# Performance work log

Hardware: AMD Instinct MI355X
Metric: run time of the kernel (lower is better)

The kernel has to match this reference:

```python
import jax, jax.numpy as jnp
import numpy as np

B, S, D = 4, 2048, 1024
P = 9            # num_paths
DM = D // 4      # bottleneck d_mid
EPS = 1e-5


def setup_inputs() -> dict:
    key = jax.random.key(0)
    ks = jax.random.split(key, 12)
    sc_in = 1.0 / np.sqrt(D)
    sc_mid = 1.0 / np.sqrt(DM)
    return {
        "x": jax.random.normal(ks[0], (B, S, D), dtype=jnp.float32),
        # neighbor mixer: per-channel 3-tap kernel over the sequence axis
        "mix_kernel": jax.random.normal(ks[1], (3, D), dtype=jnp.float32) * 0.5,
        # 9 parallel bottleneck paths: D -> D/4 -> D
        "W1": jax.random.normal(ks[2], (P, D, DM), dtype=jnp.float32) * sc_in,
        "b1": jnp.zeros((P, DM), dtype=jnp.float32),
        "W2": jax.random.normal(ks[3], (P, DM, D), dtype=jnp.float32) * sc_mid,
        "b2": jnp.zeros((P, D), dtype=jnp.float32),
        # observer: D -> D/4 -> tanh -> ... -> P scores
        "Wo1": jax.random.normal(ks[4], (D, DM), dtype=jnp.float32) * sc_in,
        "bo1": jnp.zeros((DM,), dtype=jnp.float32),
        "Wo2": jax.random.normal(ks[5], (DM, P), dtype=jnp.float32) * sc_mid,
        "bo2": jnp.zeros((P,), dtype=jnp.float32),
        # output norm affine params
        "gamma": jnp.ones((D,), dtype=jnp.float32),
        "beta": jnp.zeros((D,), dtype=jnp.float32),
    }


def _mix(x, mix_kernel):
    # eidosNeighborMixer: local 3-tap depthwise mix along sequence (non-causal)
    xp = jnp.pad(x, ((0, 0), (1, 1), (0, 0)))
    return (mix_kernel[0] * xp[:, :-2]
            + mix_kernel[1] * xp[:, 1:-1]
            + mix_kernel[2] * xp[:, 2:])


def _layernorm(h, gamma, beta):
    mu = jnp.mean(h, axis=-1, keepdims=True)
    var = jnp.var(h, axis=-1, keepdims=True)
    return (h - mu) * jax.lax.rsqrt(var + EPS) * gamma + beta


def reference(x, mix_kernel, W1, b1, W2, b2, Wo1, bo1, Wo2, bo2, gamma, beta):
    x_mixed = _mix(x, mix_kernel)                                   # [B,S,D]
    # all num_paths bottleneck transforms computed densely (as in source)
    h = jnp.einsum("bsd,pdm->bspm", x_mixed, W1) + b1               # [B,S,P,DM]
    stacked_paths = jnp.einsum("bspm,pmd->bspd", h, W2) + b2        # [B,S,P,D]
    # observer scores
    scores = jnp.tanh(x_mixed @ Wo1 + bo1) @ Wo2 + bo2              # [B,S,P]
    # eval-mode collapse: hard argmax one-hot selection
    idx = jnp.argmax(scores, axis=-1)                               # [B,S]
    weights = jax.nn.one_hot(idx, P, dtype=stacked_paths.dtype)     # [B,S,P]
    collapsed = jnp.einsum("bspd,bsp->bsd", stacked_paths, weights)  # [B,S,D]
    return _layernorm(x + collapsed, gamma, beta)
```

## Files before the change

kernel.cpp:

```cpp
#include <hip/hip_runtime.h>
#include <math.h>

#define Ss 2048
#define Dd 1024
#define Pp 9
#define DMm 256
#define Tt 8192
#define EPSf 1e-5f
#define BAND 6e-3f

typedef __attribute__((ext_vector_type(8))) __bf16 bf16x8;
typedef __attribute__((ext_vector_type(4))) float f32x4;

#define GLOBAL_AS __attribute__((address_space(1)))
#define LDS_AS __attribute__((address_space(3)))

#define MAXTILES 137

__device__ __forceinline__ unsigned short bf16rn(float f) {
  unsigned int u = __float_as_uint(f);
  unsigned int r = (u + 0x7fffu + ((u >> 16) & 1u)) >> 16;
  return (unsigned short)r;
}

__device__ __forceinline__ void gload16(const void* g, void* l) {
  __builtin_amdgcn_global_load_lds((const GLOBAL_AS unsigned int*)g,
                                   (LDS_AS unsigned int*)l, 16, 0, 0);
}

#define KSW(r, sl) (((r) << 6) + ((((sl) ^ ((r) & 7))) << 3))

__global__ __launch_bounds__(256) void k_mix2(const float* __restrict__ x,
    const float* __restrict__ mk, unsigned short* __restrict__ xh,
    int* __restrict__ counts) {
  if (blockIdx.x == 0 && threadIdx.x < 64) counts[threadIdx.x] = 0;
  const int t = blockIdx.x;
  const int s = t & (Ss - 1);
  const int d = threadIdx.x << 2;
  const float* xc = x + (size_t)t * Dd + d;
  float4 vb = *(const float4*)xc;
  float4 va = make_float4(0.f, 0.f, 0.f, 0.f);
  float4 vc = make_float4(0.f, 0.f, 0.f, 0.f);
  if (s > 0)      va = *(const float4*)(xc - Dd);
  if (s < Ss - 1) vc = *(const float4*)(xc + Dd);
  const float4 k0 = *(const float4*)(mk + d);
  const float4 k1 = *(const float4*)(mk + Dd + d);
  const float4 k2 = *(const float4*)(mk + 2 * Dd + d);
  float4 o;
  o.x = k0.x * va.x + k1.x * vb.x + k2.x * vc.x;
  o.y = k0.y * va.y + k1.y * vb.y + k2.y * vc.y;
  o.z = k0.z * va.z + k1.z * vb.z + k2.z * vc.z;
  o.w = k0.w * va.w + k1.w * vb.w + k2.w * vc.w;
  ushort4 h;
  h.x = bf16rn(o.x); h.y = bf16rn(o.y); h.z = bf16rn(o.z); h.w = bf16rn(o.w);
  *(ushort4*)(xh + (size_t)t * Dd + d) = h;
}

__global__ __launch_bounds__(256) void k_cvt_all(
    const float* __restrict__ W1, const float* __restrict__ W2,
    const float* __restrict__ Wo1,
    unsigned short* __restrict__ W1t, unsigned short* __restrict__ W2t,
    unsigned short* __restrict__ Wo1t) {
  const int z = blockIdx.z;
  const float* in; unsigned short* outp; int R, C, r0, c0;
  if (z < Pp)            { in = W1;  outp = W1t;  R = Dd;  C = DMm;
                           r0 = blockIdx.x * 32; c0 = blockIdx.y * 32; }
  else if (z < 2 * Pp)   { in = W2;  outp = W2t;  R = DMm; C = Dd;
                           r0 = blockIdx.y * 32; c0 = blockIdx.x * 32; }
  else                   { in = Wo1; outp = Wo1t; R = Dd;  C = DMm;
                           r0 = blockIdx.x * 32; c0 = blockIdx.y * 32; }
  const int zi = (z < Pp) ? z : ((z < 2 * Pp) ? z - Pp : 0);
  const size_t zo = (size_t)zi * R * C;
  __shared__ float tile[32][33];
  const int tr = threadIdx.x >> 3, tc = (threadIdx.x & 7) << 2;
  float4 v = *(const float4*)(in + zo + (size_t)(r0 + tr) * C + c0 + tc);
  tile[tr][tc] = v.x; tile[tr][tc + 1] = v.y; tile[tr][tc + 2] = v.z; tile[tr][tc + 3] = v.w;
  __syncthreads();
  ushort4 h;
  h.x = bf16rn(tile[tc + 0][tr]); h.y = bf16rn(tile[tc + 1][tr]);
  h.z = bf16rn(tile[tc + 2][tr]); h.w = bf16rn(tile[tc + 3][tr]);
  *(ushort4*)(outp + zo + (size_t)(c0 + tr) * R + r0 + tc) = h;
}

template<int KTOT, int NTOT, int MODE, bool GROUPED>
__global__ __launch_bounds__(256) void k_gemm(
    const unsigned short* __restrict__ A,
    const unsigned short* __restrict__ Bt,
    const float* __restrict__ bias,
    const float* __restrict__ resid,
    float* __restrict__ outf, unsigned short* __restrict__ outh,
    const int* __restrict__ counts, const int* __restrict__ tokenlist) {
  int p = 0, ti = blockIdx.x, cnt = Tt;
  if (GROUPED) {
    for (p = 0; p < Pp; ++p) {
      cnt = counts[p];
      const int nt = (cnt + 63) >> 6;
      if (ti < nt) break;
      ti -= nt;
    }
    if (p == Pp) return;
  }
  const int tile0 = ti * 64;
  __shared__ int tl[64];
  __shared__ __align__(16) unsigned short As[2][64 * 64];
  __shared__ __align__(16) unsigned short Bs[2][128 * 64];
  const int tid = threadIdx.x;
  if (tid < 64) {
    const int li = tile0 + tid;
    if (GROUPED) tl[tid] = (li < cnt) ? tokenlist[p * Tt + li] : tokenlist[p * Tt];
    else         tl[tid] = li;
  }
  __syncthreads();
  const int w = tid >> 6, lane = tid & 63;
  const int fr = lane & 15, fs = lane >> 4;
  const int wr = w >> 1, wc = w & 1;
  const int n0 = blockIdx.y * 128;
  const unsigned short* Bp0 = Bt + (size_t)p * NTOT * KTOT + (size_t)n0 * KTOT;
  const unsigned short* srcA[2];
  #pragma unroll
  for (int i = 0; i < 2; ++i) {
    const int u = i * 256 + tid, r = u >> 3, sl = (u & 7) ^ (r & 7);
    srcA[i] = A + (size_t)tl[r] * KTOT + sl * 8;
  }
  const unsigned short* srcB[4];
  #pragma unroll
  for (int i = 0; i < 4; ++i) {
    const int u = i * 256 + tid, r = u >> 3, sl = (u & 7) ^ (r & 7);
    srcB[i] = Bp0 + (size_t)r * KTOT + sl * 8;
  }
  const int ldsW = w * 512;
  int aoff[2][2], boff[4][2];
  #pragma unroll
  for (int m = 0; m < 2; ++m)
    #pragma unroll
    for (int kk = 0; kk < 2; ++kk)
      aoff[m][kk] = KSW(wr * 32 + m * 16 + fr, kk * 4 + fs);
  #pragma unroll
  for (int n = 0; n < 4; ++n)
    #pragma unroll
    for (int kk = 0; kk < 2; ++kk)
      boff[n][kk] = KSW(wc * 64 + n * 16 + fr, kk * 4 + fs);

#define STAGE(b, kb) do { \
    gload16(srcA[0] + (kb), &As[b][0] + ldsW); \
    gload16(srcA[1] + (kb), &As[b][0] + 2048 + ldsW); \
    gload16(srcB[0] + (kb), &Bs[b][0] + ldsW); \
    gload16(srcB[1] + (kb), &Bs[b][0] + 2048 + ldsW); \
    gload16(srcB[2] + (kb), &Bs[b][0] + 4096 + ldsW); \
    gload16(srcB[3] + (kb), &Bs[b][0] + 6144 + ldsW); \
  } while (0)

  f32x4 acc[2][4] = {};
  const int NS = KTOT / 64;
  STAGE(0, 0);
  for (int s = 0; s < NS; ++s) {
    const int buf = s & 1;
    if (s + 1 < NS) {
      STAGE(buf ^ 1, (s + 1) * 64);
      asm volatile("s_waitcnt vmcnt(6)" ::: "memory");
    } else {
      asm volatile("s_waitcnt vmcnt(0)" ::: "memory");
    }
    __builtin_amdgcn_s_barrier();
    __builtin_amdgcn_sched_barrier(0);
    const unsigned short* Ab = &As[buf][0];
    const unsigned short* Bb_ = &Bs[buf][0];
    bf16x8 a[2][2], b[4][2];
    #pragma unroll
    for (int m = 0; m < 2; ++m)
      #pragma unroll
      for (int kk = 0; kk < 2; ++kk)
        a[m][kk] = *(const bf16x8*)&Ab[aoff[m][kk]];
    #pragma unroll
    for (int n = 0; n < 4; ++n)
      #pragma unroll
      for (int kk = 0; kk < 2; ++kk)
        b[n][kk] = *(const bf16x8*)&Bb_[boff[n][kk]];
    #pragma unroll
    for (int kk = 0; kk < 2; ++kk)
      #pragma unroll
      for (int m = 0; m < 2; ++m)
        #pragma unroll
        for (int n = 0; n < 4; ++n)
          acc[m][n] = __builtin_amdgcn_mfma_f32_16x16x32_bf16(a[m][kk], b[n][kk], acc[m][n], 0, 0, 0);
    __builtin_amdgcn_s_barrier();
  }
#undef STAGE

  const float* bias_z = bias + (size_t)p * NTOT;
  #pragma unroll
  for (int m = 0; m < 2; ++m) {
    #pragma unroll
    for (int j = 0; j < 4; ++j) {
      const int rr = wr * 32 + m * 16 + fs * 4 + j;
      const int li = tile0 + rr;
      if (GROUPED && li >= cnt) continue;
      const int t = tl[rr];
      #pragma unroll
      for (int n = 0; n < 4; ++n) {
        const int c = n0 + wc * 64 + n * 16 + fr;
        const float v = acc[m][n][j] + bias_z[c];
        if (MODE == 0)      outf[(size_t)t * NTOT + c] = tanhf(v);
        else if (MODE == 1) outh[(size_t)t * NTOT + c] = bf16rn(v);
        else                outf[(size_t)t * NTOT + c] = v + resid[(size_t)t * NTOT + c];
      }
    }
  }
}

__global__ __launch_bounds__(256) void k_score(const float* __restrict__ hidden,
    const float* __restrict__ Wo2, const float* __restrict__ bo2,
    int* __restrict__ idx, int* __restrict__ nflag, int* __restrict__ flagged) {
  __shared__ float sW[DMm * Pp];
  const int tid = threadIdx.x;
  for (int l = tid; l < DMm * Pp; l += 256) sW[l] = Wo2[l];
  __syncthreads();
  const int wave = tid >> 6, lane = tid & 63;
  const int t = blockIdx.x * 4 + wave;
  const float4 h = *(const float4*)(hidden + (size_t)t * DMm + lane * 4);
  const int m = lane * 4;
  float part[Pp];
  #pragma unroll
  for (int pp = 0; pp < Pp; ++pp)
    part[pp] = h.x * sW[(m + 0) * Pp + pp] + h.y * sW[(m + 1) * Pp + pp]
             + h.z * sW[(m + 2) * Pp + pp] + h.w * sW[(m + 3) * Pp + pp];
  #pragma unroll
  for (int off = 32; off > 0; off >>= 1)
    #pragma unroll
    for (int pp = 0; pp < Pp; ++pp)
      part[pp] += __shfl_xor(part[pp], off);
  if (lane == 0) {
    float best = -1e30f, second = -1e30f;
    int bi = 0;
    #pragma unroll
    for (int pp = 0; pp < Pp; ++pp) {
      const float sc = part[pp] + bo2[pp];
      if (sc > best) { second = best; best = sc; bi = pp; }
      else if (sc > second) second = sc;
    }
    idx[t] = bi;
    if (best - second < BAND) {
      const int pos = atomicAdd(nflag, 1);
      flagged[pos] = t;
    }
  }
}

__global__ __launch_bounds__(256) void k_rescue(const float* __restrict__ x,
    const float* __restrict__ mk,
    const float* __restrict__ Wo1, const float* __restrict__ bo1,
    const float* __restrict__ Wo2, const float* __restrict__ bo2,
    const int* __restrict__ nflag, const int* __restrict__ flagged,
    int* __restrict__ idx) {
  __shared__ double sx[Dd];
  __shared__ double th[DMm];
  __shared__ double red[4][12];
  const int nf = *nflag;
  const int tid = threadIdx.x;
  const int wv = tid >> 6, ln = tid & 63;
  for (int f = blockIdx.x; f < nf; f += gridDim.x) {
    const int t = flagged[f];
    const int s = t & (Ss - 1);
    for (int l = tid; l < Dd; l += 256) {
      const double xa = (s > 0)      ? (double)x[(size_t)(t - 1) * Dd + l] : 0.0;
      const double xb =                (double)x[(size_t)t * Dd + l];
      const double xc = (s < Ss - 1) ? (double)x[(size_t)(t + 1) * Dd + l] : 0.0;
      sx[l] = (double)mk[l] * xa + (double)mk[Dd + l] * xb + (double)mk[2 * Dd + l] * xc;
    }
    __syncthreads();
    {
      double a0 = 0, a1 = 0, a2 = 0, a3 = 0;
      const float* wcol = Wo1 + tid;
      for (int d = 0; d < Dd; d += 4) {
        a0 += sx[d + 0] * (double)wcol[(size_t)(d + 0) * DMm];
        a1 += sx[d + 1] * (double)wcol[(size_t)(d + 1) * DMm];
        a2 += sx[d + 2] * (double)wcol[(size_t)(d + 2) * DMm];
        a3 += sx[d + 3] * (double)wcol[(size_t)(d + 3) * DMm];
      }
      th[tid] = tanh(((a0 + a1) + (a2 + a3)) + (double)bo1[tid]);
    }
    __syncthreads();
    double pr[Pp];
    const double tv = th[tid];
    #pragma unroll
    for (int p = 0; p < Pp; ++p) pr[p] = tv * (double)Wo2[tid * Pp + p];
    #pragma unroll
    for (int off = 32; off > 0; off >>= 1)
      #pragma unroll
      for (int p = 0; p < Pp; ++p) pr[p] += __shfl_xor(pr[p], off);
    if (ln == 0) {
      #pragma unroll
      for (int p = 0; p < Pp; ++p) red[wv][p] = pr[p];
    }
    __syncthreads();
    if (tid == 0) {
      double best = -1e300; int bi = 0;
      #pragma unroll
      for (int p = 0; p < Pp; ++p) {
        const double sv = red[0][p] + red[1][p] + red[2][p] + red[3][p] + (double)bo2[p];
        if (sv > best) { best = sv; bi = p; }
      }
      idx[t] = bi;
    }
    __syncthreads();
  }
}

__global__ __launch_bounds__(256) void k_scatter(const int* __restrict__ idx,
    int* __restrict__ counts, int* __restrict__ tokenlist) {
  __shared__ int lcnt[Pp], lbase[Pp];
  const int tid = threadIdx.x;
  if (tid < Pp) lcnt[tid] = 0;
  __syncthreads();
  const int t = blockIdx.x * 256 + tid;
  const int p = idx[t];
  const int slot = atomicAdd(&lcnt[p], 1);
  __syncthreads();
  if (tid < Pp) lbase[tid] = atomicAdd(&counts[tid], lcnt[tid]);
  __syncthreads();
  tokenlist[p * Tt + lbase[p] + slot] = t;
}

__global__ __launch_bounds__(256) void k_ln(float* __restrict__ y,
    const float* __restrict__ gamma, const float* __restrict__ beta) {
  const int t = blockIdx.x;
  const int d = threadIdx.x << 2;
  float* row = y + (size_t)t * Dd;
  float4 v = *(float4*)(row + d);
  float s = v.x + v.y + v.z + v.w;
  float q = v.x * v.x + v.y * v.y + v.z * v.z + v.w * v.w;
  #pragma unroll
  for (int off = 32; off > 0; off >>= 1) {
    s += __shfl_xor(s, off);
    q += __shfl_xor(q, off);
  }
  __shared__ float ssum[4], sqq[4];
  const int wave = threadIdx.x >> 6, lane = threadIdx.x & 63;
  if (lane == 0) { ssum[wave] = s; sqq[wave] = q; }
  __syncthreads();
  s = ssum[0] + ssum[1] + ssum[2] + ssum[3];
  q = sqq[0] + sqq[1] + sqq[2] + sqq[3];
  const float mu = s * (1.f / Dd);
  const float var = q * (1.f / Dd) - mu * mu;
  const float inv = rsqrtf(var + EPSf);
  const float4 g = *(const float4*)(gamma + d);
  const float4 bt = *(const float4*)(beta + d);
  float4 o;
  o.x = (v.x - mu) * inv * g.x + bt.x;
  o.y = (v.y - mu) * inv * g.y + bt.y;
  o.z = (v.z - mu) * inv * g.z + bt.z;
  o.w = (v.w - mu) * inv * g.w + bt.w;
  *(float4*)(row + d) = o;
}

extern "C" void kernel_launch(void* const* d_in, const int* in_sizes, int n_in,
                              void* d_out, int out_size, void* d_ws, size_t ws_size,
                              hipStream_t stream) {
  (void)in_sizes; (void)n_in; (void)out_size; (void)ws_size;
  const float* x     = (const float*)d_in[0];
  const float* mk    = (const float*)d_in[1];
  const float* W1    = (const float*)d_in[2];
  const float* b1    = (const float*)d_in[3];
  const float* W2    = (const float*)d_in[4];
  const float* b2    = (const float*)d_in[5];
  const float* Wo1   = (const float*)d_in[6];
  const float* bo1   = (const float*)d_in[7];
  const float* Wo2   = (const float*)d_in[8];
  const float* bo2   = (const float*)d_in[9];
  const float* gamma = (const float*)d_in[10];
  const float* beta  = (const float*)d_in[11];
  float* out = (float*)d_out;

  size_t off = 0;
  auto alloc = [&](size_t bytes) -> void* {
    void* p = (char*)d_ws + off;
    off += (bytes + 255) & ~(size_t)255;
    return p;
  };
  unsigned short* xm_h   = (unsigned short*)alloc((size_t)Tt * Dd * 2);
  float*          hidden = (float*)alloc((size_t)Tt * DMm * 4);
  unsigned short* h1     = (unsigned short*)hidden;
  unsigned short* W1t    = (unsigned short*)alloc((size_t)Pp * Dd * DMm * 2);
  unsigned short* W2t    = (unsigned short*)alloc((size_t)Pp * DMm * Dd * 2);
  unsigned short* Wo1t   = (unsigned short*)alloc((size_t)Dd * DMm * 2);
  int* idx      = (int*)alloc(Tt * 4);
  int* counts   = (int*)alloc(64 * 4);
  int* nflag    = counts + 16;
  int* flagged  = (int*)alloc(Tt * 4);
  int* tokenlist = (int*)alloc((size_t)Pp * Tt * 4);

  k_mix2<<<Tt, 256, 0, stream>>>(x, mk, xm_h, counts);
  k_cvt_all<<<dim3(32, 8, 2 * Pp + 1), 256, 0, stream>>>(W1, W2, Wo1, W1t, W2t, Wo1t);

  k_gemm<Dd, DMm, 0, false><<<dim3(Tt / 64, DMm / 128), 256, 0, stream>>>(
      xm_h, Wo1t, bo1, nullptr, hidden, nullptr, nullptr, nullptr);
  k_score<<<Tt / 4, 256, 0, stream>>>(hidden, Wo2, bo2, idx, nflag, flagged);
  k_rescue<<<256, 256, 0, stream>>>(x, mk, Wo1, bo1, Wo2, bo2, nflag, flagged, idx);
  k_scatter<<<Tt / 256, 256, 0, stream>>>(idx, counts, tokenlist);

  k_gemm<Dd, DMm, 1, true><<<dim3(MAXTILES, DMm / 128), 256, 0, stream>>>(
      xm_h, W1t, b1, nullptr, nullptr, h1, counts, tokenlist);
  k_gemm<DMm, Dd, 2, true><<<dim3(MAXTILES, Dd / 128), 256, 0, stream>>>(
      h1, W2t, b2, x, out, nullptr, counts, tokenlist);
  k_ln<<<Tt, 256, 0, stream>>>(out, gamma, beta);
}
```

Baseline: 146.7 us.

## Fuse second GEMM with layernorm, merge prep kernels, shrink token tiles, fold scatter into scoring

Merges the mix and weight-conversion kernels into one launch. The token scatter moves into the score and rescue kernels. The grouped GEMMs drop from 64-row to 32-row token tiles to cut padding waste per path. A new kernel computes the full 1024-wide second GEMM per 32-token tile and applies residual add plus layernorm in registers, so the fp32 intermediate round trip and the separate LN kernel go away. The cost is a much larger per-block accumulator and LDS footprint, which may lower occupancy.

```diff
diff --git a/kernel.cpp b/kernel.cpp
--- a/kernel.cpp
+++ b/kernel.cpp
@@ -15,7 +15,7 @@
 #define GLOBAL_AS __attribute__((address_space(1)))
 #define LDS_AS __attribute__((address_space(3)))
 
-#define MAXTILES 137
+#define MAXT32 (Tt / 32 + Pp)
 
 __device__ __forceinline__ unsigned short bf16rn(float f) {
   unsigned int u = __float_as_uint(f);
@@ -30,45 +30,44 @@
 
 #define KSW(r, sl) (((r) << 6) + ((((sl) ^ ((r) & 7))) << 3))
 
-__global__ __launch_bounds__(256) void k_mix2(const float* __restrict__ x,
+__global__ __launch_bounds__(256) void k_prep(const float* __restrict__ x,
     const float* __restrict__ mk, unsigned short* __restrict__ xh,
-    int* __restrict__ counts) {
-  if (blockIdx.x == 0 && threadIdx.x < 64) counts[threadIdx.x] = 0;
-  const int t = blockIdx.x;
-  const int s = t & (Ss - 1);
-  const int d = threadIdx.x << 2;
-  const float* xc = x + (size_t)t * Dd + d;
-  float4 vb = *(const float4*)xc;
-  float4 va = make_float4(0.f, 0.f, 0.f, 0.f);
-  float4 vc = make_float4(0.f, 0.f, 0.f, 0.f);
-  if (s > 0)      va = *(const float4*)(xc - Dd);
-  if (s < Ss - 1) vc = *(const float4*)(xc + Dd);
-  const float4 k0 = *(const float4*)(mk + d);
-  const float4 k1 = *(const float4*)(mk + Dd + d);
-  const float4 k2 = *(const float4*)(mk + 2 * Dd + d);
-  float4 o;
-  o.x = k0.x * va.x + k1.x * vb.x + k2.x * vc.x;
-  o.y = k0.y * va.y + k1.y * vb.y + k2.y * vc.y;
-  o.z = k0.z * va.z + k1.z * vb.z + k2.z * vc.z;
-  o.w = k0.w * va.w + k1.w * vb.w + k2.w * vc.w;
-  ushort4 h;
-  h.x = bf16rn(o.x); h.y = bf16rn(o.y); h.z = bf16rn(o.z); h.w = bf16rn(o.w);
-  *(ushort4*)(xh + (size_t)t * Dd + d) = h;
-}
-
-__global__ __launch_bounds__(256) void k_cvt_all(
     const float* __restrict__ W1, const float* __restrict__ W2,
     const float* __restrict__ Wo1,
     unsigned short* __restrict__ W1t, unsigned short* __restrict__ W2t,
-    unsigned short* __restrict__ Wo1t) {
-  const int z = blockIdx.z;
+    unsigned short* __restrict__ Wo1t, int* __restrict__ counts) {
+  const int bid = blockIdx.x;
+  if (bid < Tt) {
+    if (bid == 0 && threadIdx.x < 64) counts[threadIdx.x] = 0;
+    const int t = bid;
+    const int s = t & (Ss - 1);
+    const int d = threadIdx.x << 2;
+    const float* xc = x + (size_t)t * Dd + d;
+    float4 vb = *(const float4*)xc;
+    float4 va = make_float4(0.f, 0.f, 0.f, 0.f);
+    float4 vc = make_float4(0.f, 0.f, 0.f, 0.f);
+    if (s > 0)      va = *(const float4*)(xc - Dd);
+    if (s < Ss - 1) vc = *(const float4*)(xc + Dd);
+    const float4 k0 = *(const float4*)(mk + d);
+    const float4 k1 = *(const float4*)(mk + Dd + d);
+    const float4 k2 = *(const float4*)(mk + 2 * Dd + d);
+    float4 o;
+    o.x = k0.x * va.x + k1.x * vb.x + k2.x * vc.x;
+    o.y = k0.y * va.y + k1.y * vb.y + k2.y * vc.y;
+    o.z = k0.z * va.z + k1.z * vb.z + k2.z * vc.z;
+    o.w = k0.w * va.w + k1.w * vb.w + k2.w * vc.w;
+    ushort4 h;
+    h.x = bf16rn(o.x); h.y = bf16rn(o.y); h.z = bf16rn(o.z); h.w = bf16rn(o.w);
+    *(ushort4*)(xh + (size_t)t * Dd + d) = h;
+    return;
+  }
+  const int i = bid - Tt;
+  const int z = i >> 8, rem = i & 255;
+  const int bx = rem & 31, by = rem >> 5;
   const float* in; unsigned short* outp; int R, C, r0, c0;
-  if (z < Pp)            { in = W1;  outp = W1t;  R = Dd;  C = DMm;
-                           r0 = blockIdx.x * 32; c0 = blockIdx.y * 32; }
-  else if (z < 2 * Pp)   { in = W2;  outp = W2t;  R = DMm; C = Dd;
-                           r0 = blockIdx.y * 32; c0 = blockIdx.x * 32; }
-  else                   { in = Wo1; outp = Wo1t; R = Dd;  C = DMm;
-                           r0 = blockIdx.x * 32; c0 = blockIdx.y * 32; }
+  if (z < Pp)          { in = W1;  outp = W1t;  R = Dd;  C = DMm; r0 = bx * 32; c0 = by * 32; }
+  else if (z < 2 * Pp) { in = W2;  outp = W2t;  R = DMm; C = Dd;  r0 = by * 32; c0 = bx * 32; }
+  else                 { in = Wo1; outp = Wo1t; R = Dd;  C = DMm; r0 = bx * 32; c0 = by * 32; }
   const int zi = (z < Pp) ? z : ((z < 2 * Pp) ? z - Pp : 0);
   const size_t zo = (size_t)zi * R * C;
   __shared__ float tile[32][33];
@@ -87,25 +86,24 @@
     const unsigned short* __restrict__ A,
     const unsigned short* __restrict__ Bt,
     const float* __restrict__ bias,
-    const float* __restrict__ resid,
     float* __restrict__ outf, unsigned short* __restrict__ outh,
     const int* __restrict__ counts, const int* __restrict__ tokenlist) {
   int p = 0, ti = blockIdx.x, cnt = Tt;
   if (GROUPED) {
     for (p = 0; p < Pp; ++p) {
       cnt = counts[p];
-      const int nt = (cnt + 63) >> 6;
+      const int nt = (cnt + 31) >> 5;
       if (ti < nt) break;
       ti -= nt;
     }
     if (p == Pp) return;
   }
-  const int tile0 = ti * 64;
-  __shared__ int tl[64];
-  __shared__ __align__(16) unsigned short As[2][64 * 64];
+  const int tile0 = ti * 32;
+  __shared__ int tl[32];
+  __shared__ __align__(16) unsigned short As[2][32 * 64];
   __shared__ __align__(16) unsigned short Bs[2][128 * 64];
   const int tid = threadIdx.x;
-  if (tid < 64) {
+  if (tid < 32) {
     const int li = tile0 + tid;
     if (GROUPED) tl[tid] = (li < cnt) ? tokenlist[p * Tt + li] : tokenlist[p * Tt];
     else         tl[tid] = li;
@@ -116,12 +114,8 @@
   const int wr = w >> 1, wc = w & 1;
   const int n0 = blockIdx.y * 128;
   const unsigned short* Bp0 = Bt + (size_t)p * NTOT * KTOT + (size_t)n0 * KTOT;
-  const unsigned short* srcA[2];
-  #pragma unroll
-  for (int i = 0; i < 2; ++i) {
-    const int u = i * 256 + tid, r = u >> 3, sl = (u & 7) ^ (r & 7);
-    srcA[i] = A + (size_t)tl[r] * KTOT + sl * 8;
-  }
+  const int ua = tid, ra = ua >> 3, sa = (ua & 7) ^ (ra & 7);
+  const unsigned short* srcA = A + (size_t)tl[ra] * KTOT + sa * 8;
   const unsigned short* srcB[4];
   #pragma unroll
   for (int i = 0; i < 4; ++i) {
@@ -129,12 +123,9 @@
     srcB[i] = Bp0 + (size_t)r * KTOT + sl * 8;
   }
   const int ldsW = w * 512;
-  int aoff[2][2], boff[4][2];
-  #pragma unroll
-  for (int m = 0; m < 2; ++m)
-    #pragma unroll
-    for (int kk = 0; kk < 2; ++kk)
-      aoff[m][kk] = KSW(wr * 32 + m * 16 + fr, kk * 4 + fs);
+  int aoff[2], boff[4][2];
+  #pragma unroll
+  for (int kk = 0; kk < 2; ++kk) aoff[kk] = KSW(wr * 16 + fr, kk * 4 + fs);
   #pragma unroll
   for (int n = 0; n < 4; ++n)
     #pragma unroll
@@ -142,22 +133,21 @@
       boff[n][kk] = KSW(wc * 64 + n * 16 + fr, kk * 4 + fs);
 
 #define STAGE(b, kb) do { \
-    gload16(srcA[0] + (kb), &As[b][0] + ldsW); \
-    gload16(srcA[1] + (kb), &As[b][0] + 2048 + ldsW); \
+    gload16(srcA + (kb), &As[b][0] + ldsW); \
     gload16(srcB[0] + (kb), &Bs[b][0] + ldsW); \
     gload16(srcB[1] + (kb), &Bs[b][0] + 2048 + ldsW); \
     gload16(srcB[2] + (kb), &Bs[b][0] + 4096 + ldsW); \
     gload16(srcB[3] + (kb), &Bs[b][0] + 6144 + ldsW); \
   } while (0)
 
-  f32x4 acc[2][4] = {};
+  f32x4 acc[4] = {};
   const int NS = KTOT / 64;
   STAGE(0, 0);
   for (int s = 0; s < NS; ++s) {
     const int buf = s & 1;
     if (s + 1 < NS) {
       STAGE(buf ^ 1, (s + 1) * 64);
-      asm volatile("s_waitcnt vmcnt(6)" ::: "memory");
+      asm volatile("s_waitcnt vmcnt(5)" ::: "memory");
     } else {
       asm volatile("s_waitcnt vmcnt(0)" ::: "memory");
     }
@@ -165,12 +155,9 @@
     __builtin_amdgcn_sched_barrier(0);
     const unsigned short* Ab = &As[buf][0];
     const unsigned short* Bb_ = &Bs[buf][0];
-    bf16x8 a[2][2], b[4][2];
-    #pragma unroll
-    for (int m = 0; m < 2; ++m)
-      #pragma unroll
-      for (int kk = 0; kk < 2; ++kk)
-        a[m][kk] = *(const bf16x8*)&Ab[aoff[m][kk]];
+    bf16x8 a[2], b[4][2];
+    #pragma unroll
+    for (int kk = 0; kk < 2; ++kk) a[kk] = *(const bf16x8*)&Ab[aoff[kk]];
     #pragma unroll
     for (int n = 0; n < 4; ++n)
       #pragma unroll
@@ -179,71 +166,83 @@
     #pragma unroll
     for (int kk = 0; kk < 2; ++kk)
       #pragma unroll
-      for (int m = 0; m < 2; ++m)
-        #pragma unroll
-        for (int n = 0; n < 4; ++n)
-          acc[m][n] = __builtin_amdgcn_mfma_f32_16x16x32_bf16(a[m][kk], b[n][kk], acc[m][n], 0, 0, 0);
+      for (int n = 0; n < 4; ++n)
+        acc[n] = __builtin_amdgcn_mfma_f32_16x16x32_bf16(a[kk], b[n][kk], acc[n], 0, 0, 0);
     __builtin_amdgcn_s_barrier();
   }
 #undef STAGE
 
   const float* bias_z = bias + (size_t)p * NTOT;
   #pragma unroll
-  for (int m = 0; m < 2; ++m) {
-    #pragma unroll
-    for (int j = 0; j < 4; ++j) {
-      const int rr = wr * 32 + m * 16 + fs * 4 + j;
-      const int li = tile0 + rr;
-      if (GROUPED && li >= cnt) continue;
-      const int t = tl[rr];
-      #pragma unroll
-      for (int n = 0; n < 4; ++n) {
-        const int c = n0 + wc * 64 + n * 16 + fr;
-        const float v = acc[m][n][j] + bias_z[c];
-        if (MODE == 0)      outf[(size_t)t * NTOT + c] = tanhf(v);
-        else if (MODE == 1) outh[(size_t)t * NTOT + c] = bf16rn(v);
-        else                outf[(size_t)t * NTOT + c] = v + resid[(size_t)t * NTOT + c];
-      }
+  for (int j = 0; j < 4; ++j) {
+    const int rr = wr * 16 + fs * 4 + j;
+    const int li = tile0 + rr;
+    if (GROUPED && li >= cnt) continue;
+    const int t = tl[rr];
+    #pragma unroll
+    for (int n = 0; n < 4; ++n) {
+      const int c = n0 + wc * 64 + n * 16 + fr;
+      const float v = acc[n][j] + bias_z[c];
+      if (MODE == 0) outf[(size_t)t * NTOT + c] = tanhf(v);
+      else           outh[(size_t)t * NTOT + c] = bf16rn(v);
     }
   }
 }
 
 __global__ __launch_bounds__(256) void k_score(const float* __restrict__ hidden,
     const float* __restrict__ Wo2, const float* __restrict__ bo2,
-    int* __restrict__ idx, int* __restrict__ nflag, int* __restrict__ flagged) {
+    int* __restrict__ idx, int* __restrict__ nflag, int* __restrict__ flagged,
+    int* __restrict__ counts, int* __restrict__ tokenlist) {
   __shared__ float sW[DMm * Pp];
+  __shared__ int lcnt[Pp], lbase[Pp];
   const int tid = threadIdx.x;
   for (int l = tid; l < DMm * Pp; l += 256) sW[l] = Wo2[l];
+  if (tid < Pp) lcnt[tid] = 0;
   __syncthreads();
   const int wave = tid >> 6, lane = tid & 63;
-  const int t = blockIdx.x * 4 + wave;
-  const float4 h = *(const float4*)(hidden + (size_t)t * DMm + lane * 4);
-  const int m = lane * 4;
-  float part[Pp];
-  #pragma unroll
-  for (int pp = 0; pp < Pp; ++pp)
-    part[pp] = h.x * sW[(m + 0) * Pp + pp] + h.y * sW[(m + 1) * Pp + pp]
-             + h.z * sW[(m + 2) * Pp + pp] + h.w * sW[(m + 3) * Pp + pp];
-  #pragma unroll
-  for (int off = 32; off > 0; off >>= 1)
+  int tArr[16], pArr[16], sArr[16];
+  #pragma unroll
+  for (int it = 0; it < 16; ++it) {
+    const int t = blockIdx.x * 64 + it * 4 + wave;
+    const float4 h = *(const float4*)(hidden + (size_t)t * DMm + lane * 4);
+    const int m = lane * 4;
+    float part[Pp];
     #pragma unroll
     for (int pp = 0; pp < Pp; ++pp)
-      part[pp] += __shfl_xor(part[pp], off);
-  if (lane == 0) {
-    float best = -1e30f, second = -1e30f;
-    int bi = 0;
-    #pragma unroll
-    for (int pp = 0; pp < Pp; ++pp) {
-      const float sc = part[pp] + bo2[pp];
-      if (sc > best) { second = best; best = sc; bi = pp; }
-      else if (sc > second) second = sc;
-    }
-    idx[t] = bi;
-    if (best - second < BAND) {
-      const int pos = atomicAdd(nflag, 1);
-      flagged[pos] = t;
-    }
-  }
+      part[pp] = h.x * sW[(m + 0) * Pp + pp] + h.y * sW[(m + 1) * Pp + pp]
+               + h.z * sW[(m + 2) * Pp + pp] + h.w * sW[(m + 3) * Pp + pp];
+    #pragma unroll
+    for (int off = 32; off > 0; off >>= 1)
+      #pragma unroll
+      for (int pp = 0; pp < Pp; ++pp)
+        part[pp] += __shfl_xor(part[pp], off);
+    tArr[it] = -1;
+    if (lane == 0) {
+      float best = -1e30f, second = -1e30f;
+      int bi = 0;
+      #pragma unroll
+      for (int pp = 0; pp < Pp; ++pp) {
+        const float sc = part[pp] + bo2[pp];
+        if (sc > best) { second = best; best = sc; bi = pp; }
+        else if (sc > second) second = sc;
+      }
+      idx[t] = bi;
+      if (best - second < BAND) {
+        const int pos = atomicAdd(nflag, 1);
+        flagged[pos] = t;
+      } else {
+        tArr[it] = t; pArr[it] = bi;
+        sArr[it] = atomicAdd(&lcnt[bi], 1);
+      }
+    }
+  }
+  __syncthreads();
+  if (tid < Pp) lbase[tid] = atomicAdd(&counts[tid], lcnt[tid]);
+  __syncthreads();
+  #pragma unroll
+  for (int it = 0; it < 16; ++it)
+    if (tArr[it] >= 0)
+      tokenlist[pArr[it] * Tt + lbase[pArr[it]] + sArr[it]] = tArr[it];
 }
 
 __global__ __launch_bounds__(256) void k_rescue(const float* __restrict__ x,
@@ -251,7 +250,7 @@
     const float* __restrict__ Wo1, const float* __restrict__ bo1,
     const float* __restrict__ Wo2, const float* __restrict__ bo2,
     const int* __restrict__ nflag, const int* __restrict__ flagged,
-    int* __restrict__ idx) {
+    int* __restrict__ idx, int* __restrict__ counts, int* __restrict__ tokenlist) {
   __shared__ double sx[Dd];
   __shared__ double th[DMm];
   __shared__ double red[4][12];
@@ -301,56 +300,143 @@
         if (sv > best) { best = sv; bi = p; }
       }
       idx[t] = bi;
+      const int pos = atomicAdd(&counts[bi], 1);
+      tokenlist[bi * Tt + pos] = t;
     }
     __syncthreads();
   }
 }
 
-__global__ __launch_bounds__(256) void k_scatter(const int* __restrict__ idx,
-    int* __restrict__ counts, int* __restrict__ tokenlist) {
-  __shared__ int lcnt[Pp], lbase[Pp];
+__global__ __launch_bounds__(256) void k_g2ln(
+    const unsigned short* __restrict__ h1,
+    const unsigned short* __restrict__ W2t,
+    const float* __restrict__ b2,
+    const float* __restrict__ x,
+    const float* __restrict__ gamma, const float* __restrict__ beta,
+    const int* __restrict__ counts, const int* __restrict__ tokenlist,
+    float* __restrict__ out) {
+  int p = 0, ti = blockIdx.x, cnt = 0;
+  for (p = 0; p < Pp; ++p) {
+    cnt = counts[p];
+    const int nt = (cnt + 31) >> 5;
+    if (ti < nt) break;
+    ti -= nt;
+  }
+  if (p == Pp) return;
+  const int tile0 = ti * 32;
+  __shared__ int tl[32];
+  __shared__ __align__(16) unsigned short Bs[2][64 * 256];
+  __shared__ float sS[32][2], sQ[32][2];
   const int tid = threadIdx.x;
-  if (tid < Pp) lcnt[tid] = 0;
-  __syncthreads();
-  const int t = blockIdx.x * 256 + tid;
-  const int p = idx[t];
-  const int slot = atomicAdd(&lcnt[p], 1);
-  __syncthreads();
-  if (tid < Pp) lbase[tid] = atomicAdd(&counts[tid], lcnt[tid]);
-  __syncthreads();
-  tokenlist[p * Tt + lbase[p] + slot] = t;
-}
-
-__global__ __launch_bounds__(256) void k_ln(float* __restrict__ y,
-    const float* __restrict__ gamma, const float* __restrict__ beta) {
-  const int t = blockIdx.x;
-  const int d = threadIdx.x << 2;
-  float* row = y + (size_t)t * Dd;
-  float4 v = *(float4*)(row + d);
-  float s = v.x + v.y + v.z + v.w;
-  float q = v.x * v.x + v.y * v.y + v.z * v.z + v.w * v.w;
-  #pragma unroll
-  for (int off = 32; off > 0; off >>= 1) {
-    s += __shfl_xor(s, off);
-    q += __shfl_xor(q, off);
-  }
-  __shared__ float ssum[4], sqq[4];
-  const int wave = threadIdx.x >> 6, lane = threadIdx.x & 63;
-  if (lane == 0) { ssum[wave] = s; sqq[wave] = q; }
-  __syncthreads();
-  s = ssum[0] + ssum[1] + ssum[2] + ssum[3];
-  q = sqq[0] + sqq[1] + sqq[2] + sqq[3];
-  const float mu = s * (1.f / Dd);
-  const float var = q * (1.f / Dd) - mu * mu;
-  const float inv = rsqrtf(var + EPSf);
-  const float4 g = *(const float4*)(gamma + d);
-  const float4 bt = *(const float4*)(beta + d);
-  float4 o;
-  o.x = (v.x - mu) * inv * g.x + bt.x;
-  o.y = (v.y - mu) * inv * g.y + bt.y;
-  o.z = (v.z - mu) * inv * g.z + bt.z;
-  o.w = (v.w - mu) * inv * g.w + bt.w;
-  *(float4*)(row + d) = o;
+  if (tid < 32) {
+    const int li = tile0 + tid;
+    tl[tid] = (li < cnt) ? tokenlist[p * Tt + li] : tokenlist[p * Tt];
+  }
+  __syncthreads();
+  const int w = tid >> 6, lane = tid & 63;
+  const int fr = lane & 15, fs = lane >> 4;
+  const int th = w >> 1, ch = w & 1;
+  const unsigned short* arow = h1 + (size_t)tl[th * 16 + fr] * DMm;
+  bf16x8 pa[8];
+  #pragma unroll
+  for (int ks = 0; ks < 8; ++ks) pa[ks] = *(const bf16x8*)(arow + ks * 32 + fs * 8);
+  const unsigned short* Bbase = W2t + (size_t)p * Dd * DMm;
+  int srow[8], ssl[8];
+  #pragma unroll
+  for (int i = 0; i < 8; ++i) {
+    const int u = i * 256 + tid;
+    srow[i] = u >> 5;
+    ssl[i] = ((u & 31) ^ (srow[i] & 31)) << 3;
+  }
+#define STG(b, cb) do { \
+    unsigned short* L = &Bs[b][0]; \
+    _Pragma("unroll") \
+    for (int i = 0; i < 8; ++i) \
+      gload16(Bbase + (size_t)((cb) + srow[i]) * DMm + ssl[i], L + (i * 256 + tid) * 8); \
+  } while (0)
+
+  f32x4 acc[16][2] = {};
+  STG(0, 0);
+  STG(1, 64);
+  #pragma unroll
+  for (int c = 0; c < 16; ++c) {
+    const int buf = c & 1;
+    if (c < 15) asm volatile("s_waitcnt vmcnt(8)" ::: "memory");
+    else        asm volatile("s_waitcnt vmcnt(0)" ::: "memory");
+    __builtin_amdgcn_s_barrier();
+    __builtin_amdgcn_sched_barrier(0);
+    #pragma unroll
+    for (int ks = 0; ks < 8; ++ks) {
+      #pragma unroll
+      for (int nf = 0; nf < 2; ++nf) {
+        const int rc = ch * 32 + nf * 16 + fr;
+        const bf16x8 bfrag = *(const bf16x8*)&Bs[buf][rc * 256 + ((((ks * 4 + fs)) ^ (rc & 31)) << 3)];
+        acc[c][nf] = __builtin_amdgcn_mfma_f32_16x16x32_bf16(pa[ks], bfrag, acc[c][nf], 0, 0, 0);
+      }
+    }
+    __builtin_amdgcn_s_barrier();
+    if (c + 2 < 16) STG(buf, (c + 2) * 64);
+  }
+#undef STG
+
+  const float* b2p = b2 + (size_t)p * Dd;
+  int tok[4];
+  #pragma unroll
+  for (int j = 0; j < 4; ++j) tok[j] = tl[th * 16 + fs * 4 + j];
+  float s[4] = {}, q[4] = {};
+  #pragma unroll
+  for (int c = 0; c < 16; ++c) {
+    #pragma unroll
+    for (int nf = 0; nf < 2; ++nf) {
+      const int col = c * 64 + ch * 32 + nf * 16 + fr;
+      const float bv = b2p[col];
+      #pragma unroll
+      for (int j = 0; j < 4; ++j) {
+        const float h = acc[c][nf][j] + bv + x[(size_t)tok[j] * Dd + col];
+        acc[c][nf][j] = h;
+        s[j] += h; q[j] += h * h;
+      }
+    }
+  }
+  #pragma unroll
+  for (int off = 1; off < 16; off <<= 1)
+    #pragma unroll
+    for (int j = 0; j < 4; ++j) {
+      s[j] += __shfl_xor(s[j], off);
+      q[j] += __shfl_xor(q[j], off);
+    }
+  if (fr == 0) {
+    #pragma unroll
+    for (int j = 0; j < 4; ++j) {
+      sS[th * 16 + fs * 4 + j][ch] = s[j];
+      sQ[th * 16 + fs * 4 + j][ch] = q[j];
+    }
+  }
+  __syncthreads();
+  float mu[4], inv[4];
+  #pragma unroll
+  for (int j = 0; j < 4; ++j) {
+    const int r = th * 16 + fs * 4 + j;
+    const float S = sS[r][0] + sS[r][1];
+    const float Q = sQ[r][0] + sQ[r][1];
+    mu[j] = S * (1.f / Dd);
+    const float var = Q * (1.f / Dd) - mu[j] * mu[j];
+    inv[j] = rsqrtf(var + EPSf);
+  }
+  #pragma unroll
+  for (int c = 0; c < 16; ++c) {
+    #pragma unroll
+    for (int nf = 0; nf < 2; ++nf) {
+      const int col = c * 64 + ch * 32 + nf * 16 + fr;
+      const float g = gamma[col], bt = beta[col];
+      #pragma unroll
+      for (int j = 0; j < 4; ++j) {
+        const int li = tile0 + th * 16 + fs * 4 + j;
+        if (li >= cnt) continue;
+        out[(size_t)tok[j] * Dd + col] = (acc[c][nf][j] - mu[j]) * inv[j] * g + bt;
+      }
+    }
+  }
 }
 
 extern "C" void kernel_launch(void* const* d_in, const int* in_sizes, int n_in,
@@ -389,18 +475,18 @@
   int* flagged  = (int*)alloc(Tt * 4);
   int* tokenlist = (int*)alloc((size_t)Pp * Tt * 4);
 
-  k_mix2<<<Tt, 256, 0, stream>>>(x, mk, xm_h, counts);
-  k_cvt_all<<<dim3(32, 8, 2 * Pp + 1), 256, 0, stream>>>(W1, W2, Wo1, W1t, W2t, Wo1t);
-
-  k_gemm<Dd, DMm, 0, false><<<dim3(Tt / 64, DMm / 128), 256, 0, stream>>>(
-      xm_h, Wo1t, bo1, nullptr, hidden, nullptr, nullptr, nullptr);
-  k_score<<<Tt / 4, 256, 0, stream>>>(hidden, Wo2, bo2, idx, nflag, flagged);
-  k_rescue<<<256, 256, 0, stream>>>(x, mk, Wo1, bo1, Wo2, bo2, nflag, flagged, idx);
-  k_scatter<<<Tt / 256, 256, 0, stream>>>(idx, counts, tokenlist);
-
-  k_gemm<Dd, DMm, 1, true><<<dim3(MAXTILES, DMm / 128), 256, 0, stream>>>(
-      xm_h, W1t, b1, nullptr, nullptr, h1, counts, tokenlist);
-  k_gemm<DMm, Dd, 2, true><<<dim3(MAXTILES, Dd / 128), 256, 0, stream>>>(
-      h1, W2t, b2, x, out, nullptr, counts, tokenlist);
-  k_ln<<<Tt, 256, 0, stream>>>(out, gamma, beta);
-}
+  k_prep<<<Tt + (2 * Pp + 1) * 256, 256, 0, stream>>>(
+      x, mk, xm_h, W1, W2, Wo1, W1t, W2t, Wo1t, counts);
+
+  k_gemm<Dd, DMm, 0, false><<<dim3(Tt / 32, DMm / 128), 256, 0, stream>>>(
+      xm_h, Wo1t, bo1, hidden, nullptr, nullptr, nullptr);
+  k_score<<<Tt / 64, 256, 0, stream>>>(hidden, Wo2, bo2, idx, nflag, flagged,
+                                       counts, tokenlist);
+  k_rescue<<<256, 256, 0, stream>>>(x, mk, Wo1, bo1, Wo2, bo2, nflag, flagged,
+                                    idx, counts, tokenlist);
+
+  k_gemm<Dd, DMm, 1, true><<<dim3(MAXT32, DMm / 128), 256, 0, stream>>>(
+      xm_h, W1t, b1, nullptr, h1, counts, tokenlist);
+  k_g2ln<<<MAXT32, 256, 0, stream>>>(h1, W2t, b2, x, gamma, beta,
+                                     counts, tokenlist, out);
+}
```

New measurement: 162.4 us. +10.7%, slower.
